# Kernel optimization log

Hardware: AMD Instinct MI355X
Metric: run time of the kernel (lower is better)

## Reference

```python
import jax, jax.numpy as jnp
import numpy as np

BATCH = 1024
MAX_LEN = 200
MAX_K = 8
IN_U = 256
OUT_U = 256
ITERATION = 3
NEG_PAD = jnp.float32(-2.0**16 + 1)  # -65535, same as torch code


def squash(x):
    # NOTE: torch code sums over dim=1, which here is the capsule (max_K) axis.
    vec_sq_norm = jnp.sum(jnp.square(x), axis=1, keepdims=True)
    scale = vec_sq_norm / (1.0 + vec_sq_norm) / jnp.sqrt(vec_sq_norm + 1e-9)
    return scale * x


def setup_inputs() -> dict:
    key = jax.random.key(0)
    k1, k2, k3, k4 = jax.random.split(key, 4)
    low_capsule = jax.random.normal(k1, (BATCH, MAX_LEN, IN_U), dtype=jnp.float32)
    seq_len = jax.random.randint(k2, (BATCH, 1), 0, MAX_LEN)  # values < max_len per assert
    S_matrix = jax.random.normal(k3, (IN_U, OUT_U), dtype=jnp.float32)
    B_matrix = jax.random.normal(k4, (1, MAX_K, MAX_LEN), dtype=jnp.float32)
    return {"low_capsule": low_capsule, "S_matrix": S_matrix,
            "B_matrix": B_matrix, "seq_len": seq_len}


def reference(low_capsule, S_matrix, B_matrix, seq_len):
    # mask: [B,1,L], broadcasts against B_matrix [1,K,L] -> [B,K,L]
    mask = jnp.arange(MAX_LEN)[None, None, :] < seq_len[:, :, None]
    # loop-invariant projection (torch recomputes identically each iteration)
    low_new = jnp.einsum('ble,eo->blo', low_capsule, S_matrix)  # [B,L,O]
    Bm = B_matrix
    high = None
    for _ in range(ITERATION):
        logits = jnp.where(mask, Bm, NEG_PAD)          # [B,K,L]
        W = jax.nn.softmax(logits, axis=-1)            # [B,K,L]
        high = squash(jnp.einsum('bkl,blo->bko', W, low_new))  # [B,K,O]
        B_delta = jnp.sum(jnp.einsum('bko,blo->bkl', high, low_new),
                          axis=0, keepdims=True)       # [1,K,L]
        Bm = Bm + B_delta
    return high
```

## Files before the change

kernel.cpp:

```cpp
#include <hip/hip_runtime.h>

#define BATCH   1024
#define MAXLEN  200
#define KCAPS   8
#define INU     256
#define OUTU    256
#define NEGPAD  -65535.0f
#define HSTR    264

typedef _Float16 f16;
typedef _Float16 f16x8 __attribute__((ext_vector_type(8)));
typedef float    f32x4 __attribute__((ext_vector_type(4)));
typedef float    f32x2 __attribute__((ext_vector_type(2)));

__global__ void k_prep(const float* __restrict__ S, const float* __restrict__ Bm,
                       f16* __restrict__ Shi, f16* __restrict__ Slo,
                       f16* __restrict__ Thi, f16* __restrict__ Tlo,
                       float* __restrict__ Bcur) {
    int idx = blockIdx.x * 256 + threadIdx.x;
    if (idx < KCAPS * MAXLEN) Bcur[idx] = Bm[idx];
    int j    = idx & 7;
    int lane = (idx >> 3) & 63;
    int nf   = (idx >> 9) & 15;
    int ks   = idx >> 13;
    int k = ks * 32 + (lane >> 4) * 8 + j;
    int n = nf * 16 + (lane & 15);
    float vS = S[k * 256 + n];
    f16 hS = (f16)vS;
    Shi[idx] = hS;
    Slo[idx] = (f16)(vS - (float)hS);
    float vT = S[n * 256 + k];
    f16 hT = (f16)vT;
    Thi[idx] = hT;
    Tlo[idx] = (f16)(vT - (float)hT);
}

#define EFRAG(MF, ACC) do {                                                          \
    const int l_  = (MF) * 16 + r15;                                                 \
    const int lc_ = (l_ < MAXLEN) ? l_ : (MAXLEN - 1);                               \
    const float* ap_ = lb + (size_t)lc_ * INU + q * 8;                               \
    f32x4 va[8], vb[8];                                                              \
    _Pragma("unroll")                                                                \
    for (int ks = 0; ks < 8; ks++) {                                                 \
        va[ks] = *reinterpret_cast<const f32x4*>(ap_ + ks * 32);                     \
        vb[ks] = *reinterpret_cast<const f32x4*>(ap_ + ks * 32 + 4);                 \
    }                                                                                \
    _Pragma("unroll")                                                                \
    for (int ks = 0; ks < 8; ks++) {                                                 \
        const int ob_ = ks * 32 + q * 8;                                             \
        f32x4 h0 = *reinterpret_cast<const f32x4*>(&GH[r15 * HSTR + ob_]);           \
        f32x4 h1 = *reinterpret_cast<const f32x4*>(&GH[r15 * HSTR + ob_ + 4]);       \
        f16x8 bh, bl, ah, al;                                                        \
        _Pragma("unroll")                                                            \
        for (int j = 0; j < 4; j++) { f16 t = (f16)h0[j]; bh[j] = t; bl[j] = (f16)(h0[j] - (float)t); } \
        _Pragma("unroll")                                                            \
        for (int j = 0; j < 4; j++) { f16 t = (f16)h1[j]; bh[4+j] = t; bl[4+j] = (f16)(h1[j] - (float)t); } \
        _Pragma("unroll")                                                            \
        for (int j = 0; j < 4; j++) { f16 t = (f16)va[ks][j]; ah[j] = t; al[j] = (f16)(va[ks][j] - (float)t); } \
        _Pragma("unroll")                                                            \
        for (int j = 0; j < 4; j++) { f16 t = (f16)vb[ks][j]; ah[4+j] = t; al[4+j] = (f16)(vb[ks][j] - (float)t); } \
        ACC = __builtin_amdgcn_mfma_f32_16x16x32_f16(ah, bh, ACC, 0, 0, 0);          \
        ACC = __builtin_amdgcn_mfma_f32_16x16x32_f16(al, bh, ACC, 0, 0, 0);          \
        ACC = __builtin_amdgcn_mfma_f32_16x16x32_f16(ah, bl, ACC, 0, 0, 0);          \
    }                                                                                \
} while (0)

__global__ __launch_bounds__(512, 4) void k_G(const float* __restrict__ Bcur,
                                              const int*   __restrict__ seq_len,
                                              const float* __restrict__ low,
                                              const f16*   __restrict__ Shi,
                                              const f16*   __restrict__ Slo,
                                              const f16*   __restrict__ Thi,
                                              const f16*   __restrict__ Tlo,
                                              float*       __restrict__ partials,
                                              float*       __restrict__ out,
                                              int do_T) {
    __shared__ float Wl[KCAPS * MAXLEN];
    __shared__ float GH[16 * HSTR];
    __shared__ float Sl2[2 * KCAPS * 256];
    const int b   = blockIdx.x;
    const int tid = threadIdx.x;
    const int len = seq_len[b];

    for (int i = tid; i < KCAPS * MAXLEN; i += 512) Wl[i] = Bcur[i];
    for (int i = tid; i < 16 * HSTR; i += 512) GH[i] = 0.f;
    __syncthreads();

    {
        const int k  = tid >> 6;
        const int ln = tid & 63;
        float m = -3.4e38f;
        for (int l = ln; l < MAXLEN; l += 64) {
            float v = (l < len) ? Wl[k * MAXLEN + l] : NEGPAD;
            m = fmaxf(m, v);
        }
        #pragma unroll
        for (int off = 32; off >= 1; off >>= 1) m = fmaxf(m, __shfl_xor(m, off));
        float ssum = 0.f;
        for (int l = ln; l < MAXLEN; l += 64) {
            float v = (l < len) ? Wl[k * MAXLEN + l] : NEGPAD;
            ssum += __expf(v - m);
        }
        #pragma unroll
        for (int off = 32; off >= 1; off >>= 1) ssum += __shfl_xor(ssum, off);
        float inv = 1.f / ssum;
        for (int l = ln; l < MAXLEN; l += 64) {
            float v = (l < len) ? Wl[k * MAXLEN + l] : NEGPAD;
            Wl[k * MAXLEN + l] = __expf(v - m) * inv;
        }
    }
    __syncthreads();

    const float* lb = low + (size_t)b * (MAXLEN * INU);

    {
        const int cp = tid & 127;
        const int rg = tid >> 7;
        const int lim = (len == 0) ? MAXLEN : len;
        const float* cb = lb + cp * 2;
        f32x2 g[KCAPS];
        #pragma unroll
        for (int k = 0; k < KCAPS; k++) g[k] = (f32x2){0.f, 0.f};
        int l = rg;
        for (; l + 4 < lim; l += 8) {
            f32x2 va = *reinterpret_cast<const f32x2*>(cb + l * INU);
            f32x2 vb = *reinterpret_cast<const f32x2*>(cb + (l + 4) * INU);
            #pragma unroll
            for (int k = 0; k < KCAPS; k++) {
                float wa = Wl[k * MAXLEN + l];
                float wb = Wl[k * MAXLEN + l + 4];
                g[k][0] = fmaf(wa, va[0], g[k][0]);
                g[k][1] = fmaf(wa, va[1], g[k][1]);
                g[k][0] = fmaf(wb, vb[0], g[k][0]);
                g[k][1] = fmaf(wb, vb[1], g[k][1]);
            }
        }
        if (l < lim) {
            f32x2 va = *reinterpret_cast<const f32x2*>(cb + l * INU);
            #pragma unroll
            for (int k = 0; k < KCAPS; k++) {
                float wa = Wl[k * MAXLEN + l];
                g[k][0] = fmaf(wa, va[0], g[k][0]);
                g[k][1] = fmaf(wa, va[1], g[k][1]);
            }
        }
        if (rg >= 2) {
            #pragma unroll
            for (int k = 0; k < KCAPS; k++)
                *reinterpret_cast<f32x2*>(&Sl2[((rg - 2) * KCAPS + k) * 256 + cp * 2]) = g[k];
        }
        __syncthreads();
        if (rg == 1) {
            #pragma unroll
            for (int k = 0; k < KCAPS; k++) {
                f32x2 t = *reinterpret_cast<f32x2*>(&Sl2[(KCAPS + k) * 256 + cp * 2]);
                g[k][0] += t[0]; g[k][1] += t[1];
                *reinterpret_cast<f32x2*>(&Sl2[(KCAPS + k) * 256 + cp * 2]) = g[k];
            }
        } else if (rg == 0) {
            #pragma unroll
            for (int k = 0; k < KCAPS; k++) {
                f32x2 t = *reinterpret_cast<f32x2*>(&Sl2[k * 256 + cp * 2]);
                g[k][0] += t[0]; g[k][1] += t[1];
            }
        }
        __syncthreads();
        if (rg == 0) {
            #pragma unroll
            for (int k = 0; k < KCAPS; k++) {
                f32x2 t = *reinterpret_cast<f32x2*>(&Sl2[(KCAPS + k) * 256 + cp * 2]);
                GH[k * HSTR + cp * 2]     = g[k][0] + t[0];
                GH[k * HSTR + cp * 2 + 1] = g[k][1] + t[1];
            }
        }
    }
    __syncthreads();

    const int wv = tid >> 6, lane = tid & 63;
    const int r15 = lane & 15, q = lane >> 4;
    f32x4 aC[2];
    aC[0] = (f32x4){0.f, 0.f, 0.f, 0.f};
    aC[1] = (f32x4){0.f, 0.f, 0.f, 0.f};
    #pragma unroll
    for (int ks = 0; ks < 8; ks++) {
        const float* gp = &GH[r15 * HSTR + ks * 32 + q * 8];
        f32x4 a0 = *reinterpret_cast<const f32x4*>(gp);
        f32x4 a1 = *reinterpret_cast<const f32x4*>(gp + 4);
        f16x8 ah, al;
        #pragma unroll
        for (int j = 0; j < 4; j++) {
            f16 t = (f16)a0[j]; ah[j] = t; al[j] = (f16)(a0[j] - (float)t);
        }
        #pragma unroll
        for (int j = 0; j < 4; j++) {
            f16 t = (f16)a1[j]; ah[4 + j] = t; al[4 + j] = (f16)(a1[j] - (float)t);
        }
        #pragma unroll
        for (int i = 0; i < 2; i++) {
            const int nf = wv * 2 + i;
            f16x8 bh = *reinterpret_cast<const f16x8*>(Shi + (ks * 16 + nf) * 512 + lane * 8);
            f16x8 bl = *reinterpret_cast<const f16x8*>(Slo + (ks * 16 + nf) * 512 + lane * 8);
            aC[i] = __builtin_amdgcn_mfma_f32_16x16x32_f16(ah, bh, aC[i], 0, 0, 0);
            aC[i] = __builtin_amdgcn_mfma_f32_16x16x32_f16(al, bh, aC[i], 0, 0, 0);
            aC[i] = __builtin_amdgcn_mfma_f32_16x16x32_f16(ah, bl, aC[i], 0, 0, 0);
        }
    }
    float s0, s1;
    {
        float n0 = aC[0][0]*aC[0][0] + aC[0][1]*aC[0][1] + aC[0][2]*aC[0][2] + aC[0][3]*aC[0][3];
        float n1 = aC[1][0]*aC[1][0] + aC[1][1]*aC[1][1] + aC[1][2]*aC[1][2] + aC[1][3]*aC[1][3];
        n0 += __shfl_xor(n0, 16);
        n1 += __shfl_xor(n1, 16);
        s0 = n0 / (1.f + n0) * (1.f / sqrtf(n0 + 1e-9f));
        s1 = n1 / (1.f + n1) * (1.f / sqrtf(n1 + 1e-9f));
    }
    if (!do_T) {
        if (q < 2) {
            #pragma unroll
            for (int r = 0; r < 4; r++) {
                out[((size_t)b * KCAPS + q * 4 + r) * OUTU + (wv * 2 + 0) * 16 + r15] = s0 * aC[0][r];
                out[((size_t)b * KCAPS + q * 4 + r) * OUTU + (wv * 2 + 1) * 16 + r15] = s1 * aC[1][r];
            }
        }
        return;
    }
    __syncthreads();
    if (q < 2) {
        #pragma unroll
        for (int r = 0; r < 4; r++) {
            GH[(q * 4 + r) * HSTR + (wv * 2 + 0) * 16 + r15] = s0 * aC[0][r];
            GH[(q * 4 + r) * HSTR + (wv * 2 + 1) * 16 + r15] = s1 * aC[1][r];
        }
    }
    __syncthreads();

    f32x4 aD[2];
    aD[0] = (f32x4){0.f, 0.f, 0.f, 0.f};
    aD[1] = (f32x4){0.f, 0.f, 0.f, 0.f};
    #pragma unroll
    for (int ks = 0; ks < 8; ks++) {
        const float* hp = &GH[r15 * HSTR + ks * 32 + q * 8];
        f32x4 a0 = *reinterpret_cast<const f32x4*>(hp);
        f32x4 a1 = *reinterpret_cast<const f32x4*>(hp + 4);
        f16x8 ah, al;
        #pragma unroll
        for (int j = 0; j < 4; j++) {
            f16 t = (f16)a0[j]; ah[j] = t; al[j] = (f16)(a0[j] - (float)t);
        }
        #pragma unroll
        for (int j = 0; j < 4; j++) {
            f16 t = (f16)a1[j]; ah[4 + j] = t; al[4 + j] = (f16)(a1[j] - (float)t);
        }
        #pragma unroll
        for (int i = 0; i < 2; i++) {
            const int nf = wv * 2 + i;
            f16x8 bh = *reinterpret_cast<const f16x8*>(Thi + (ks * 16 + nf) * 512 + lane * 8);
            f16x8 bl = *reinterpret_cast<const f16x8*>(Tlo + (ks * 16 + nf) * 512 + lane * 8);
            aD[i] = __builtin_amdgcn_mfma_f32_16x16x32_f16(ah, bh, aD[i], 0, 0, 0);
            aD[i] = __builtin_amdgcn_mfma_f32_16x16x32_f16(al, bh, aD[i], 0, 0, 0);
            aD[i] = __builtin_amdgcn_mfma_f32_16x16x32_f16(ah, bl, aD[i], 0, 0, 0);
        }
    }
    __syncthreads();
    if (q < 2) {
        #pragma unroll
        for (int r = 0; r < 4; r++) {
            GH[(q * 4 + r) * HSTR + (wv * 2 + 0) * 16 + r15] = aD[0][r];
            GH[(q * 4 + r) * HSTR + (wv * 2 + 1) * 16 + r15] = aD[1][r];
        }
    }
    __syncthreads();

    f32x4 accA = (f32x4){0.f, 0.f, 0.f, 0.f};
    f32x4 accB = (f32x4){0.f, 0.f, 0.f, 0.f};
    EFRAG(wv, accA);
    if (wv < 5) EFRAG(wv + 8, accB);

    if (r15 < KCAPS) {
        const int kcol = r15;
        float* pb = partials + (size_t)b * (KCAPS * MAXLEN);
        {
            const int lbase = wv * 16 + q * 4;
            #pragma unroll
            for (int r = 0; r < 4; r++)
                pb[(lbase + r) * KCAPS + kcol] = accA[r];
        }
        if (wv < 5) {
            const int lbase = (wv + 8) * 16 + q * 4;
            #pragma unroll
            for (int r = 0; r < 4; r++) {
                const int l = lbase + r;
                if (l < MAXLEN)
                    pb[l * KCAPS + kcol] = accB[r];
            }
        }
    }
}

__global__ __launch_bounds__(256) void k_update(const float* __restrict__ partials,
                                                float* __restrict__ Bcur) {
    __shared__ float red[256];
    const int j   = blockIdx.x;
    const int tid = threadIdx.x;
    float s = 0.f;
    #pragma unroll
    for (int jj = 0; jj < BATCH / 256; jj++)
        s += partials[(size_t)(tid + jj * 256) * (KCAPS * MAXLEN) + j];
    red[tid] = s;
    __syncthreads();
    for (int st = 128; st > 0; st >>= 1) {
        if (tid < st) red[tid] += red[tid + st];
        __syncthreads();
    }
    if (tid == 0) Bcur[(j & 7) * MAXLEN + (j >> 3)] += red[0];
}

extern "C" void kernel_launch(void* const* d_in, const int* in_sizes, int n_in,
                              void* d_out, int out_size, void* d_ws, size_t ws_size,
                              hipStream_t stream) {
    const float* low = (const float*)d_in[0];
    const float* S   = (const float*)d_in[1];
    const float* Bm  = (const float*)d_in[2];
    const int*   seq = (const int*)d_in[3];
    float* out = (float*)d_out;

    char* ws = (char*)d_ws;
    float* Bcur     = (float*)ws;
    float* partials = (float*)(ws + 6400);
    f16*   Shi      = (f16*)(ws + 6560000);
    f16*   Slo      = (f16*)(ws + 6691072);
    f16*   Thi      = (f16*)(ws + 6822144);
    f16*   Tlo      = (f16*)(ws + 6953216);

    k_prep<<<256, 256, 0, stream>>>(S, Bm, Shi, Slo, Thi, Tlo, Bcur);
    for (int it = 0; it < 3; it++) {
        int last = (it == 2);
        k_G<<<BATCH, 512, 0, stream>>>(Bcur, seq, low, Shi, Slo, Thi, Tlo,
                                       partials, out, last ? 0 : 1);
        if (!last) k_update<<<KCAPS * MAXLEN, 256, 0, stream>>>(partials, Bcur);
    }
}
```

Baseline: 211.1 us.

## Restructure weighted row sum into per-wave full-row accumulation with MFMA-folded reduction

Replaces the 4-group, length-limited weighted sum of input rows. Each wave now handles an interleaved set of all 200 rows, loading float4 columns eight rows at a time to keep more loads in flight. The eight per-wave partials are merged into two 8-row banks of the shared tile through serialized synchronized steps. The two banks are summed after the first MFMA with a cross-lane shuffle, which removes the extra shared scratch buffer and its zeroing. The trade-off is that every row is read regardless of the sequence length, so the masked padding rows, which previously were skipped, now add memory traffic.

```diff
diff --git a/kernel.cpp b/kernel.cpp
--- a/kernel.cpp
+++ b/kernel.cpp
@@ -11,7 +11,6 @@
 typedef _Float16 f16;
 typedef _Float16 f16x8 __attribute__((ext_vector_type(8)));
 typedef float    f32x4 __attribute__((ext_vector_type(4)));
-typedef float    f32x2 __attribute__((ext_vector_type(2)));
 
 __global__ void k_prep(const float* __restrict__ S, const float* __restrict__ Bm,
                        f16* __restrict__ Shi, f16* __restrict__ Slo,
@@ -77,13 +76,11 @@
                                               int do_T) {
     __shared__ float Wl[KCAPS * MAXLEN];
     __shared__ float GH[16 * HSTR];
-    __shared__ float Sl2[2 * KCAPS * 256];
     const int b   = blockIdx.x;
     const int tid = threadIdx.x;
     const int len = seq_len[b];
 
     for (int i = tid; i < KCAPS * MAXLEN; i += 512) Wl[i] = Bcur[i];
-    for (int i = tid; i < 16 * HSTR; i += 512) GH[i] = 0.f;
     __syncthreads();
 
     {
@@ -112,72 +109,67 @@
     __syncthreads();
 
     const float* lb = low + (size_t)b * (MAXLEN * INU);
-
-    {
-        const int cp = tid & 127;
-        const int rg = tid >> 7;
-        const int lim = (len == 0) ? MAXLEN : len;
-        const float* cb = lb + cp * 2;
-        f32x2 g[KCAPS];
-        #pragma unroll
-        for (int k = 0; k < KCAPS; k++) g[k] = (f32x2){0.f, 0.f};
-        int l = rg;
-        for (; l + 4 < lim; l += 8) {
-            f32x2 va = *reinterpret_cast<const f32x2*>(cb + l * INU);
-            f32x2 vb = *reinterpret_cast<const f32x2*>(cb + (l + 4) * INU);
-            #pragma unroll
-            for (int k = 0; k < KCAPS; k++) {
-                float wa = Wl[k * MAXLEN + l];
-                float wb = Wl[k * MAXLEN + l + 4];
-                g[k][0] = fmaf(wa, va[0], g[k][0]);
-                g[k][1] = fmaf(wa, va[1], g[k][1]);
-                g[k][0] = fmaf(wb, vb[0], g[k][0]);
-                g[k][1] = fmaf(wb, vb[1], g[k][1]);
-            }
-        }
-        if (l < lim) {
-            f32x2 va = *reinterpret_cast<const f32x2*>(cb + l * INU);
-            #pragma unroll
-            for (int k = 0; k < KCAPS; k++) {
-                float wa = Wl[k * MAXLEN + l];
-                g[k][0] = fmaf(wa, va[0], g[k][0]);
-                g[k][1] = fmaf(wa, va[1], g[k][1]);
-            }
-        }
-        if (rg >= 2) {
-            #pragma unroll
-            for (int k = 0; k < KCAPS; k++)
-                *reinterpret_cast<f32x2*>(&Sl2[((rg - 2) * KCAPS + k) * 256 + cp * 2]) = g[k];
-        }
-        __syncthreads();
-        if (rg == 1) {
-            #pragma unroll
-            for (int k = 0; k < KCAPS; k++) {
-                f32x2 t = *reinterpret_cast<f32x2*>(&Sl2[(KCAPS + k) * 256 + cp * 2]);
-                g[k][0] += t[0]; g[k][1] += t[1];
-                *reinterpret_cast<f32x2*>(&Sl2[(KCAPS + k) * 256 + cp * 2]) = g[k];
-            }
-        } else if (rg == 0) {
-            #pragma unroll
-            for (int k = 0; k < KCAPS; k++) {
-                f32x2 t = *reinterpret_cast<f32x2*>(&Sl2[k * 256 + cp * 2]);
-                g[k][0] += t[0]; g[k][1] += t[1];
-            }
-        }
-        __syncthreads();
-        if (rg == 0) {
-            #pragma unroll
-            for (int k = 0; k < KCAPS; k++) {
-                f32x2 t = *reinterpret_cast<f32x2*>(&Sl2[(KCAPS + k) * 256 + cp * 2]);
-                GH[k * HSTR + cp * 2]     = g[k][0] + t[0];
-                GH[k * HSTR + cp * 2 + 1] = g[k][1] + t[1];
-            }
-        }
-    }
-    __syncthreads();
-
     const int wv = tid >> 6, lane = tid & 63;
     const int r15 = lane & 15, q = lane >> 4;
+
+    {
+        const float* cb = lb + lane * 4;
+        f32x4 g[KCAPS];
+        #pragma unroll
+        for (int k = 0; k < KCAPS; k++) g[k] = (f32x4){0.f, 0.f, 0.f, 0.f};
+        #pragma unroll
+        for (int jb = 0; jb < 3; jb++) {
+            f32x4 v[8];
+            #pragma unroll
+            for (int u = 0; u < 8; u++)
+                v[u] = *reinterpret_cast<const f32x4*>(cb + (size_t)(wv + (jb * 8 + u) * 8) * INU);
+            #pragma unroll
+            for (int u = 0; u < 8; u++) {
+                const int l = wv + (jb * 8 + u) * 8;
+                #pragma unroll
+                for (int k = 0; k < KCAPS; k++) {
+                    const float w = Wl[k * MAXLEN + l];
+                    g[k][0] = fmaf(w, v[u][0], g[k][0]);
+                    g[k][1] = fmaf(w, v[u][1], g[k][1]);
+                    g[k][2] = fmaf(w, v[u][2], g[k][2]);
+                    g[k][3] = fmaf(w, v[u][3], g[k][3]);
+                }
+            }
+        }
+        {
+            const int l = wv + 192;
+            f32x4 v = *reinterpret_cast<const f32x4*>(cb + (size_t)l * INU);
+            #pragma unroll
+            for (int k = 0; k < KCAPS; k++) {
+                const float w = Wl[k * MAXLEN + l];
+                g[k][0] = fmaf(w, v[0], g[k][0]);
+                g[k][1] = fmaf(w, v[1], g[k][1]);
+                g[k][2] = fmaf(w, v[2], g[k][2]);
+                g[k][3] = fmaf(w, v[3], g[k][3]);
+            }
+        }
+        const int bank = wv & 1;
+        const int step = wv >> 1;
+        #pragma unroll
+        for (int s = 0; s < 4; s++) {
+            if (step == s) {
+                if (s == 0) {
+                    #pragma unroll
+                    for (int k = 0; k < KCAPS; k++)
+                        *reinterpret_cast<f32x4*>(&GH[(bank * 8 + k) * HSTR + lane * 4]) = g[k];
+                } else {
+                    #pragma unroll
+                    for (int k = 0; k < KCAPS; k++) {
+                        float* p = &GH[(bank * 8 + k) * HSTR + lane * 4];
+                        f32x4 t = *reinterpret_cast<const f32x4*>(p);
+                        *reinterpret_cast<f32x4*>(p) = t + g[k];
+                    }
+                }
+            }
+            __syncthreads();
+        }
+    }
+
     f32x4 aC[2];
     aC[0] = (f32x4){0.f, 0.f, 0.f, 0.f};
     aC[1] = (f32x4){0.f, 0.f, 0.f, 0.f};
@@ -207,6 +199,10 @@
     }
     float s0, s1;
     {
+        #pragma unroll
+        for (int i = 0; i < 2; i++)
+            #pragma unroll
+            for (int r = 0; r < 4; r++) aC[i][r] += __shfl_xor(aC[i][r], 32);
         float n0 = aC[0][0]*aC[0][0] + aC[0][1]*aC[0][1] + aC[0][2]*aC[0][2] + aC[0][3]*aC[0][3];
         float n1 = aC[1][0]*aC[1][0] + aC[1][1]*aC[1][1] + aC[1][2]*aC[1][2] + aC[1][3]*aC[1][3];
         n0 += __shfl_xor(n0, 16);
@@ -225,12 +221,10 @@
         return;
     }
     __syncthreads();
-    if (q < 2) {
-        #pragma unroll
-        for (int r = 0; r < 4; r++) {
-            GH[(q * 4 + r) * HSTR + (wv * 2 + 0) * 16 + r15] = s0 * aC[0][r];
-            GH[(q * 4 + r) * HSTR + (wv * 2 + 1) * 16 + r15] = s1 * aC[1][r];
-        }
+    #pragma unroll
+    for (int r = 0; r < 4; r++) {
+        GH[(q * 4 + r) * HSTR + (wv * 2 + 0) * 16 + r15] = (q < 2) ? s0 * aC[0][r] : 0.f;
+        GH[(q * 4 + r) * HSTR + (wv * 2 + 1) * 16 + r15] = (q < 2) ? s1 * aC[1][r] : 0.f;
     }
     __syncthreads();
 
@@ -262,12 +256,10 @@
         }
     }
     __syncthreads();
-    if (q < 2) {
-        #pragma unroll
-        for (int r = 0; r < 4; r++) {
-            GH[(q * 4 + r) * HSTR + (wv * 2 + 0) * 16 + r15] = aD[0][r];
-            GH[(q * 4 + r) * HSTR + (wv * 2 + 1) * 16 + r15] = aD[1][r];
-        }
+    #pragma unroll
+    for (int r = 0; r < 4; r++) {
+        GH[(q * 4 + r) * HSTR + (wv * 2 + 0) * 16 + r15] = (q < 2) ? aD[0][r] : 0.f;
+        GH[(q * 4 + r) * HSTR + (wv * 2 + 1) * 16 + r15] = (q < 2) ? aD[1][r] : 0.f;
     }
     __syncthreads();
 
```

Measured after the change: 242.9 us. +15.1%, slower.
